# Optimization experiments

Measured on AMD Instinct MI355X. Metric: run time of the kernel, lower is better.

Reference implementation:

```python
import jax, jax.numpy as jnp
import numpy as np

E = 1024   # d_model
H = 16     # nhead
F = 4096   # dim_feedforward
EPS = 1e-5


def _ln(x, g, b):
    mu = jnp.mean(x, axis=-1, keepdims=True)
    var = jnp.mean(jnp.square(x - mu), axis=-1, keepdims=True)
    return (x - mu) * jax.lax.rsqrt(var + EPS) * g + b


def setup_inputs() -> dict:
    key = jax.random.key(0)
    ks = jax.random.split(key, 12)
    s = 0.02
    return {
        "query": jax.random.normal(ks[0], (4, 512, E), jnp.float32),
        "key_value": jax.random.normal(ks[1], (4, 2048, E), jnp.float32),
        "wq": jax.random.normal(ks[2], (E, E), jnp.float32) * s,
        "wk": jax.random.normal(ks[3], (E, E), jnp.float32) * s,
        "wv": jax.random.normal(ks[4], (E, E), jnp.float32) * s,
        "bq": jnp.zeros((E,), jnp.float32),
        "bk": jnp.zeros((E,), jnp.float32),
        "bv": jnp.zeros((E,), jnp.float32),
        "wo": jax.random.normal(ks[5], (E, E), jnp.float32) * s,
        "bo": jnp.zeros((E,), jnp.float32),
        "g1": jnp.ones((E,), jnp.float32),
        "be1": jnp.zeros((E,), jnp.float32),
        "w1": jax.random.normal(ks[6], (F, E), jnp.float32) * s,
        "b1": jnp.zeros((F,), jnp.float32),
        "w2": jax.random.normal(ks[7], (E, F), jnp.float32) * s,
        "b2": jnp.zeros((E,), jnp.float32),
        "g2": jnp.ones((E,), jnp.float32),
        "be2": jnp.zeros((E,), jnp.float32),
    }


def reference(query, key_value, wq, wk, wv, bq, bk, bv, wo, bo,
              g1, be1, w1, b1, w2, b2, g2, be2):
    B, Lq, _ = query.shape
    Lk = key_value.shape[1]
    Dh = E // H
    # projections (torch Linear: x @ W.T + b)
    q = (query @ wq.T + bq).reshape(B, Lq, H, Dh).transpose(0, 2, 1, 3)   # bhqd
    k = (key_value @ wk.T + bk).reshape(B, Lk, H, Dh).transpose(0, 2, 1, 3)
    v = (key_value @ wv.T + bv).reshape(B, Lk, H, Dh).transpose(0, 2, 1, 3)
    scores = jnp.einsum('bhqd,bhkd->bhqk', q, k) / jnp.sqrt(jnp.float32(Dh))
    attn = jax.nn.softmax(scores, axis=-1)                                # [B,H,Lq,Lk]
    ctx = jnp.einsum('bhqk,bhkd->bhqd', attn, v)
    ctx = ctx.transpose(0, 2, 1, 3).reshape(B, Lq, E)
    attn_out = ctx @ wo.T + bo
    # residual + LN1 (dropout = 0)
    q2 = _ln(query + attn_out, g1, be1)
    # FFN (ReLU activation per default)
    ffn = jax.nn.relu(q2 @ w1.T + b1) @ w2.T + b2
    q3 = _ln(q2 + ffn, g2, be2)
    return q3, attn
```

## Files before the change

kernel.cpp:

```cpp
#include <hip/hip_runtime.h>
#include <hip/hip_bf16.h>

#define E_DIM 1024
#define NHEAD 16
#define DHEAD 64
#define FDIM 4096
#define LQ 512
#define LKV 2048
#define NB 4

typedef __bf16 bfx8 __attribute__((ext_vector_type(8)));
typedef float f32x4 __attribute__((ext_vector_type(4)));
typedef unsigned short us8 __attribute__((ext_vector_type(8)));
typedef unsigned short us4 __attribute__((ext_vector_type(4)));

__device__ __forceinline__ unsigned short f2bf(float f){
  union { float f; unsigned int u; } v; v.f = f;
  unsigned int u = v.u;
  u += 0x7FFFu + ((u >> 16) & 1u);
  return (unsigned short)(u >> 16);
}

__device__ __forceinline__ float fexp2(float x){
#if __has_builtin(__builtin_amdgcn_exp2f)
  return __builtin_amdgcn_exp2f(x);
#else
  return exp2f(x);
#endif
}

__global__ __launch_bounds__(256) void cvt_kernel(const float* __restrict__ src,
                                                  unsigned short* __restrict__ dst){
  size_t i = ((size_t)blockIdx.x * 256 + threadIdx.x) * 8;
  float4 a = *reinterpret_cast<const float4*>(src + i);
  float4 b = *reinterpret_cast<const float4*>(src + i + 4);
  us8 o;
  o[0]=f2bf(a.x); o[1]=f2bf(a.y); o[2]=f2bf(a.z); o[3]=f2bf(a.w);
  o[4]=f2bf(b.x); o[5]=f2bf(b.y); o[6]=f2bf(b.z); o[7]=f2bf(b.w);
  *reinterpret_cast<us8*>(dst + i) = o;
}

template<int BN, bool HASBIAS, bool RELU, bool OUTF, bool OUTB>
__global__ __launch_bounds__(256) void gemm128(
    const unsigned short* __restrict__ A, const unsigned short* __restrict__ W,
    const float* __restrict__ bias, float* __restrict__ Cf, unsigned short* __restrict__ Cb,
    int M, int N, int K, int lda, int ldw, int ldc)
{
  constexpr int BM  = 128;
  constexpr int NFB = BN / 32;
  __shared__ unsigned short As[BM * 64];
  __shared__ unsigned short Bs[BN * 64];

  const int tid = threadIdx.x, lane = tid & 63, w = tid >> 6;
  const int wr = w >> 1, wc = w & 1;
  const int m0 = blockIdx.y * BM, n0 = blockIdx.x * BN;
  const int l15 = lane & 15, l4 = lane >> 4;

  f32x4 acc[4][NFB] = {};

  for (int k0 = 0; k0 < K; k0 += 64){
    __syncthreads();
    #pragma unroll
    for (int c = 0; c < BM/32; c++){
      const int o = (c*256 + tid) * 16;
      const int row = o >> 7, colb = o & 127;
      __builtin_amdgcn_global_load_lds(
        (const __attribute__((address_space(1))) void*)
            ((const char*)A + ((long)(m0+row)*lda + k0)*2 + colb),
        (__attribute__((address_space(3))) unsigned int*)((char*)As + o), 16, 0, 0);
    }
    #pragma unroll
    for (int c = 0; c < BN/32; c++){
      const int o = (c*256 + tid) * 16;
      const int row = o >> 7, colb = o & 127;
      __builtin_amdgcn_global_load_lds(
        (const __attribute__((address_space(1))) void*)
            ((const char*)W + ((long)(n0+row)*ldw + k0)*2 + colb),
        (__attribute__((address_space(3))) unsigned int*)((char*)Bs + o), 16, 0, 0);
    }
    __syncthreads();
    #pragma unroll
    for (int kk = 0; kk < 2; kk++){
      const int kb = kk*32 + l4*8;
      bfx8 af[4], bf[NFB];
      #pragma unroll
      for (int mi = 0; mi < 4; mi++)
        af[mi] = *reinterpret_cast<const bfx8*>(&As[(wr*64 + mi*16 + l15)*64 + kb]);
      #pragma unroll
      for (int ni = 0; ni < NFB; ni++)
        bf[ni] = *reinterpret_cast<const bfx8*>(&Bs[(wc*(BN/2) + ni*16 + l15)*64 + kb]);
      #pragma unroll
      for (int mi = 0; mi < 4; mi++)
        #pragma unroll
        for (int ni = 0; ni < NFB; ni++)
          acc[mi][ni] = __builtin_amdgcn_mfma_f32_16x16x32_bf16(af[mi], bf[ni], acc[mi][ni], 0,0,0);
    }
  }

  const int rbase = m0 + wr*64 + l4*4;
  const int cbase = n0 + wc*(BN/2) + l15;
  #pragma unroll
  for (int mi = 0; mi < 4; mi++)
  #pragma unroll
  for (int ni = 0; ni < NFB; ni++){
    const int nn = cbase + ni*16;
    float bv = 0.f;
    if constexpr (HASBIAS) bv = bias[nn];
    #pragma unroll
    for (int r = 0; r < 4; r++){
      const int mm = rbase + mi*16 + r;
      float v = acc[mi][ni][r];
      if constexpr (HASBIAS) v += bv;
      if constexpr (RELU) v = fmaxf(v, 0.f);
      const long idx = (long)mm*ldc + nn;
      if constexpr (OUTF) Cf[idx] = v;
      if constexpr (OUTB) Cb[idx] = f2bf(v);
    }
  }
}

__global__ __launch_bounds__(256) void transpose_v_kernel(const unsigned short* __restrict__ vp,
                                                          unsigned short* __restrict__ vt){
  __shared__ unsigned short T[128][66];
  const int z = blockIdx.x; const int b = z >> 4, h = z & 15;
  const int lk0 = blockIdx.y * 128;
  const int tid = threadIdx.x;
  #pragma unroll
  for (int c = 0; c < 4; c++){
    int ch = tid + c*256;
    int row = ch >> 3, col = (ch & 7) << 3;
    us8 v = *reinterpret_cast<const us8*>(vp + (long)b*LKV*E_DIM + (long)(lk0+row)*E_DIM + h*DHEAD + col);
    #pragma unroll
    for (int j = 0; j < 8; j++) T[row][col+j] = v[j];
  }
  __syncthreads();
  #pragma unroll
  for (int c = 0; c < 4; c++){
    int ch = tid + c*256;
    int d = ch >> 4, lkc = (ch & 15) << 3;
    us8 o;
    #pragma unroll
    for (int j = 0; j < 8; j++) o[j] = T[lkc+j][d];
    *reinterpret_cast<us8*>(vt + (long)z*DHEAD*LKV + (long)d*LKV + lk0 + lkc) = o;
  }
}

__global__ __launch_bounds__(256) void attn_fused(
    const unsigned short* __restrict__ qp, const unsigned short* __restrict__ kp,
    const unsigned short* __restrict__ vt, float* __restrict__ probs,
    unsigned short* __restrict__ ctx)
{
  __shared__ unsigned short Pl[4][2][16][72];

  const int hw = blockIdx.x;
  const int logical = (hw & 7)*64 + (hw >> 3);
  const int head = logical >> 3, qt = logical & 7;
  const int b = head >> 4, h = head & 15;

  const int tid = threadIdx.x, lane = tid & 63, w = tid >> 6;
  const int l15 = lane & 15, l4 = lane >> 4;
  const float SC = 0.18033688011112042f;

  const unsigned short* qb = qp + ((long)(b*LQ + qt*64 + w*16 + l15))*E_DIM + h*DHEAD + l4*8;
  bfx8 qf[2];
  qf[0] = *reinterpret_cast<const bfx8*>(qb);
  qf[1] = *reinterpret_cast<const bfx8*>(qb + 32);

  const unsigned short* kb = kp + ((long)(b*LKV) + l15)*E_DIM + h*DHEAD + l4*8;
  const unsigned short* vb = vt + ((long)head)*DHEAD*LKV + (long)l15*LKV + l4*8;

  float mloc[4] = {-1e30f,-1e30f,-1e30f,-1e30f};
  float psum[4] = {0.f,0.f,0.f,0.f};

  for (int kt = 0; kt < LKV/64; kt++){
    f32x4 s[4] = {};
    #pragma unroll
    for (int kk = 0; kk < 2; kk++)
      #pragma unroll
      for (int nf = 0; nf < 4; nf++){
        bfx8 kf = *reinterpret_cast<const bfx8*>(kb + ((long)(kt*64 + nf*16))*E_DIM + kk*32);
        s[nf] = __builtin_amdgcn_mfma_f32_16x16x32_bf16(qf[kk], kf, s[nf], 0,0,0);
      }
    #pragma unroll
    for (int r = 0; r < 4; r++){
      float nm = mloc[r];
      float e0 = s[0][r]*SC, e1 = s[1][r]*SC, e2 = s[2][r]*SC, e3 = s[3][r]*SC;
      nm = fmaxf(nm, fmaxf(fmaxf(e0,e1), fmaxf(e2,e3)));
      float add = fexp2(e0-nm) + fexp2(e1-nm) + fexp2(e2-nm) + fexp2(e3-nm);
      psum[r] = psum[r]*fexp2(mloc[r]-nm) + add;
      mloc[r] = nm;
    }
  }
  float m2[4], linv[4];
  #pragma unroll
  for (int r = 0; r < 4; r++){
    float m = mloc[r];
    m = fmaxf(m, __shfl_xor(m, 1)); m = fmaxf(m, __shfl_xor(m, 2));
    m = fmaxf(m, __shfl_xor(m, 4)); m = fmaxf(m, __shfl_xor(m, 8));
    float p = psum[r] * fexp2(mloc[r] - m);
    p += __shfl_xor(p, 1); p += __shfl_xor(p, 2);
    p += __shfl_xor(p, 4); p += __shfl_xor(p, 8);
    m2[r] = m; linv[r] = 1.f / p;
  }

  f32x4 pv[4] = {};
  float* prow = probs + ((long)head*LQ + qt*64 + w*16 + l4*4)*LKV + l15;
  for (int kt = 0; kt < LKV/64; kt++){
    f32x4 s[4] = {};
    #pragma unroll
    for (int kk = 0; kk < 2; kk++)
      #pragma unroll
      for (int nf = 0; nf < 4; nf++){
        bfx8 kf = *reinterpret_cast<const bfx8*>(kb + ((long)(kt*64 + nf*16))*E_DIM + kk*32);
        s[nf] = __builtin_amdgcn_mfma_f32_16x16x32_bf16(qf[kk], kf, s[nf], 0,0,0);
      }
    const int par = kt & 1;
    #pragma unroll
    for (int nf = 0; nf < 4; nf++)
      #pragma unroll
      for (int r = 0; r < 4; r++){
        float pr = fexp2(s[nf][r]*SC - m2[r]) * linv[r];
        prow[(long)r*LKV + kt*64 + nf*16] = pr;
        Pl[w][par][l4*4+r][nf*16+l15] = f2bf(pr);
      }
    #pragma unroll
    for (int kk = 0; kk < 2; kk++){
      bfx8 pa = *reinterpret_cast<const bfx8*>(&Pl[w][par][l15][kk*32 + l4*8]);
      #pragma unroll
      for (int nf = 0; nf < 4; nf++){
        bfx8 vf = *reinterpret_cast<const bfx8*>(vb + (long)(nf*16)*LKV + kt*64 + kk*32);
        pv[nf] = __builtin_amdgcn_mfma_f32_16x16x32_bf16(pa, vf, pv[nf], 0,0,0);
      }
    }
  }
  unsigned short* crow = ctx + ((long)(b*LQ + qt*64 + w*16 + l4*4))*E_DIM + h*DHEAD + l15;
  #pragma unroll
  for (int nf = 0; nf < 4; nf++)
    #pragma unroll
    for (int r = 0; r < 4; r++)
      crow[(long)r*E_DIM + nf*16] = f2bf(pv[nf][r]);
}

template<bool OUTB>
__global__ __launch_bounds__(256) void ln_kernel(
    const float* __restrict__ X, const float* __restrict__ Y,
    const float* __restrict__ g, const float* __restrict__ be,
    float* __restrict__ outF, unsigned short* __restrict__ outBp)
{
  __shared__ float redA[4], redB[4];
  const long base = (long)blockIdx.x * E_DIM;
  const int tid = threadIdx.x;
  float4 x = *reinterpret_cast<const float4*>(X + base + tid*4);
  float4 y = *reinterpret_cast<const float4*>(Y + base + tid*4);
  x.x += y.x; x.y += y.y; x.z += y.z; x.w += y.w;
  float s1 = x.x + x.y + x.z + x.w;
  float s2 = x.x*x.x + x.y*x.y + x.z*x.z + x.w*x.w;
  #pragma unroll
  for (int off = 32; off; off >>= 1){ s1 += __shfl_xor(s1, off); s2 += __shfl_xor(s2, off); }
  if ((tid & 63) == 0){ redA[tid>>6] = s1; redB[tid>>6] = s2; }
  __syncthreads();
  s1 = redA[0]+redA[1]+redA[2]+redA[3];
  s2 = redB[0]+redB[1]+redB[2]+redB[3];
  const float mean = s1 * (1.0f/E_DIM);
  const float var  = s2 * (1.0f/E_DIM) - mean*mean;
  const float inv  = rsqrtf(var + 1e-5f);
  float4 gv = *reinterpret_cast<const float4*>(g  + tid*4);
  float4 bv = *reinterpret_cast<const float4*>(be + tid*4);
  float4 o;
  o.x = (x.x - mean)*inv*gv.x + bv.x;
  o.y = (x.y - mean)*inv*gv.y + bv.y;
  o.z = (x.z - mean)*inv*gv.z + bv.z;
  o.w = (x.w - mean)*inv*gv.w + bv.w;
  *reinterpret_cast<float4*>(outF + base + tid*4) = o;
  if constexpr (OUTB){
    us4 ob; ob[0]=f2bf(o.x); ob[1]=f2bf(o.y); ob[2]=f2bf(o.z); ob[3]=f2bf(o.w);
    *reinterpret_cast<us4*>(outBp + base + tid*4) = ob;
  }
}

extern "C" void kernel_launch(void* const* d_in, const int* in_sizes, int n_in,
                              void* d_out, int out_size, void* d_ws, size_t ws_size,
                              hipStream_t stream)
{
  const float* query     = (const float*)d_in[0];
  const float* key_value = (const float*)d_in[1];
  const float* wq = (const float*)d_in[2];
  const float* wk = (const float*)d_in[3];
  const float* wv = (const float*)d_in[4];
  const float* bq = (const float*)d_in[5];
  const float* bk = (const float*)d_in[6];
  const float* bv = (const float*)d_in[7];
  const float* wo = (const float*)d_in[8];
  const float* bo = (const float*)d_in[9];
  const float* g1 = (const float*)d_in[10];
  const float* be1= (const float*)d_in[11];
  const float* w1 = (const float*)d_in[12];
  const float* b1 = (const float*)d_in[13];
  const float* w2 = (const float*)d_in[14];
  const float* b2 = (const float*)d_in[15];
  const float* g2 = (const float*)d_in[16];
  const float* be2= (const float*)d_in[17];

  float* q3   = (float*)d_out;
  float* attn = q3 + (size_t)NB*LQ*E_DIM;

  unsigned short* u = (unsigned short*)d_ws;
  unsigned short* xq_b  = u; u += 2097152;
  unsigned short* xkv_b = u; u += 8388608;
  unsigned short* wq_b  = u; u += 1048576;
  unsigned short* wk_b  = u; u += 1048576;
  unsigned short* wv_b  = u; u += 1048576;
  unsigned short* wo_b  = u; u += 1048576;
  unsigned short* w1_b  = u; u += 4194304;
  unsigned short* w2_b  = u; u += 4194304;
  unsigned short* qp_b  = u; u += 2097152;
  unsigned short* kp_b  = u; u += 8388608;
  unsigned short* vp_b  = u; u += 8388608;
  unsigned short* vt_b  = u; u += 8388608;
  unsigned short* ctx_b = u; u += 2097152;
  unsigned short* q2_b  = u; u += 2097152;
  float* attn_out_f = (float*)xkv_b;
  float* q2_f       = (float*)kp_b;
  float* ffn_f      = (float*)vp_b;
  unsigned short* h1_b = vt_b;

  const dim3 blk(256);

  cvt_kernel<<<dim3(1024), blk, 0, stream>>>(query, xq_b);
  cvt_kernel<<<dim3(4096), blk, 0, stream>>>(key_value, xkv_b);
  cvt_kernel<<<dim3(512),  blk, 0, stream>>>(wq, wq_b);
  cvt_kernel<<<dim3(512),  blk, 0, stream>>>(wk, wk_b);
  cvt_kernel<<<dim3(512),  blk, 0, stream>>>(wv, wv_b);
  cvt_kernel<<<dim3(512),  blk, 0, stream>>>(wo, wo_b);
  cvt_kernel<<<dim3(2048), blk, 0, stream>>>(w1, w1_b);
  cvt_kernel<<<dim3(2048), blk, 0, stream>>>(w2, w2_b);

  gemm128<64 ,true,false,false,true><<<dim3(16,16), blk, 0, stream>>>(
      xq_b, wq_b, bq, nullptr, qp_b, NB*LQ, E_DIM, E_DIM, E_DIM, E_DIM, E_DIM);
  gemm128<128,true,false,false,true><<<dim3(8,64), blk, 0, stream>>>(
      xkv_b, wk_b, bk, nullptr, kp_b, NB*LKV, E_DIM, E_DIM, E_DIM, E_DIM, E_DIM);
  gemm128<128,true,false,false,true><<<dim3(8,64), blk, 0, stream>>>(
      xkv_b, wv_b, bv, nullptr, vp_b, NB*LKV, E_DIM, E_DIM, E_DIM, E_DIM, E_DIM);

  transpose_v_kernel<<<dim3(NB*NHEAD, LKV/128), blk, 0, stream>>>(vp_b, vt_b);

  attn_fused<<<dim3(512), blk, 0, stream>>>(qp_b, kp_b, vt_b, attn, ctx_b);

  gemm128<64,true,false,true,false><<<dim3(16,16), blk, 0, stream>>>(
      ctx_b, wo_b, bo, attn_out_f, nullptr, NB*LQ, E_DIM, E_DIM, E_DIM, E_DIM, E_DIM);

  ln_kernel<true><<<dim3(NB*LQ), blk, 0, stream>>>(query, attn_out_f, g1, be1, q2_f, q2_b);

  gemm128<128,true,true,false,true><<<dim3(32,16), blk, 0, stream>>>(
      q2_b, w1_b, b1, nullptr, h1_b, NB*LQ, FDIM, E_DIM, E_DIM, E_DIM, FDIM);

  gemm128<64,true,false,true,false><<<dim3(16,16), blk, 0, stream>>>(
      h1_b, w2_b, b2, ffn_f, nullptr, NB*LQ, E_DIM, FDIM, FDIM, FDIM, E_DIM);

  ln_kernel<false><<<dim3(NB*LQ), blk, 0, stream>>>(q2_f, ffn_f, g2, be2, q3, nullptr);
}
```

Before: 770.2 us.

## Split attention key range across four wave groups with split-K softmax merge

The attention kernel now runs 1024 threads per block: 16 waves, where four groups each handle a quarter of the key/value sequence for the same 64 query rows. Per-group running max and sum are exchanged through shared memory to build the global softmax statistics, and the partial PV accumulators are reduced through shared memory, aliased onto the P buffer, before writing ctx. This is meant to raise parallelism and latency hiding in a kernel that had only 512 blocks of 4 waves. In exchange it adds barriers and shared-memory reductions, and the larger block may limit registers per thread.

New measurement: 765.8 us. About the same (-0.6%).

```diff
diff --git a/kernel.cpp b/kernel.cpp
--- a/kernel.cpp
+++ b/kernel.cpp
@@ -145,12 +145,15 @@
   }
 }
 
-__global__ __launch_bounds__(256) void attn_fused(
+__global__ __launch_bounds__(1024) void attn_fused(
     const unsigned short* __restrict__ qp, const unsigned short* __restrict__ kp,
     const unsigned short* __restrict__ vt, float* __restrict__ probs,
     unsigned short* __restrict__ ctx)
 {
-  __shared__ unsigned short Pl[4][2][16][72];
+  __shared__ unsigned short Pl[16][2][16][72];
+  __shared__ float MLm[16][16];
+  __shared__ float MLl[16][16];
+  float (*PVm)[16][64] = (float (*)[16][64])(void*)Pl;
 
   const int hw = blockIdx.x;
   const int logical = (hw & 7)*64 + (hw >> 3);
@@ -158,10 +161,12 @@
   const int b = head >> 4, h = head & 15;
 
   const int tid = threadIdx.x, lane = tid & 63, w = tid >> 6;
+  const int wq = w & 3, ws = w >> 2;
   const int l15 = lane & 15, l4 = lane >> 4;
+  const int kt0 = ws*8, kt1 = kt0 + 8;
   const float SC = 0.18033688011112042f;
 
-  const unsigned short* qb = qp + ((long)(b*LQ + qt*64 + w*16 + l15))*E_DIM + h*DHEAD + l4*8;
+  const unsigned short* qb = qp + ((long)(b*LQ + qt*64 + wq*16 + l15))*E_DIM + h*DHEAD + l4*8;
   bfx8 qf[2];
   qf[0] = *reinterpret_cast<const bfx8*>(qb);
   qf[1] = *reinterpret_cast<const bfx8*>(qb + 32);
@@ -172,7 +177,7 @@
   float mloc[4] = {-1e30f,-1e30f,-1e30f,-1e30f};
   float psum[4] = {0.f,0.f,0.f,0.f};
 
-  for (int kt = 0; kt < LKV/64; kt++){
+  for (int kt = kt0; kt < kt1; kt++){
     f32x4 s[4] = {};
     #pragma unroll
     for (int kk = 0; kk < 2; kk++)
@@ -191,7 +196,6 @@
       mloc[r] = nm;
     }
   }
-  float m2[4], linv[4];
   #pragma unroll
   for (int r = 0; r < 4; r++){
     float m = mloc[r];
@@ -200,12 +204,24 @@
     float p = psum[r] * fexp2(mloc[r] - m);
     p += __shfl_xor(p, 1); p += __shfl_xor(p, 2);
     p += __shfl_xor(p, 4); p += __shfl_xor(p, 8);
-    m2[r] = m; linv[r] = 1.f / p;
+    if (l15 == 0){ MLm[w][l4*4+r] = m; MLl[w][l4*4+r] = p; }
+  }
+  __syncthreads();
+  float m2[4], linv[4];
+  #pragma unroll
+  for (int r = 0; r < 4; r++){
+    const int row = l4*4 + r;
+    float ma = MLm[wq   ][row], mb2 = MLm[wq+ 4][row];
+    float mc = MLm[wq+ 8][row], md  = MLm[wq+12][row];
+    float mg = fmaxf(fmaxf(ma,mb2), fmaxf(mc,md));
+    float lg = MLl[wq   ][row]*fexp2(ma -mg) + MLl[wq+ 4][row]*fexp2(mb2-mg)
+             + MLl[wq+ 8][row]*fexp2(mc -mg) + MLl[wq+12][row]*fexp2(md -mg);
+    m2[r] = mg; linv[r] = 1.f / lg;
   }
 
   f32x4 pv[4] = {};
-  float* prow = probs + ((long)head*LQ + qt*64 + w*16 + l4*4)*LKV + l15;
-  for (int kt = 0; kt < LKV/64; kt++){
+  float* prow = probs + ((long)head*LQ + qt*64 + wq*16 + l4*4)*LKV + l15;
+  for (int kt = kt0; kt < kt1; kt++){
     f32x4 s[4] = {};
     #pragma unroll
     for (int kk = 0; kk < 2; kk++)
@@ -233,12 +249,35 @@
       }
     }
   }
-  unsigned short* crow = ctx + ((long)(b*LQ + qt*64 + w*16 + l4*4))*E_DIM + h*DHEAD + l15;
-  #pragma unroll
-  for (int nf = 0; nf < 4; nf++)
-    #pragma unroll
-    for (int r = 0; r < 4; r++)
-      crow[(long)r*E_DIM + nf*16] = f2bf(pv[nf][r]);
+
+  __syncthreads();
+  if (ws != 0){
+    const int i = (ws-1)*4 + wq;
+    #pragma unroll
+    for (int nf = 0; nf < 4; nf++)
+      #pragma unroll
+      for (int r = 0; r < 4; r++)
+        PVm[i][l4*4+r][nf*16+l15] = pv[nf][r];
+  }
+  __syncthreads();
+  if (ws == 0){
+    #pragma unroll
+    for (int nf = 0; nf < 4; nf++)
+      #pragma unroll
+      for (int r = 0; r < 4; r++){
+        float v = pv[nf][r];
+        v += PVm[wq  ][l4*4+r][nf*16+l15];
+        v += PVm[wq+4][l4*4+r][nf*16+l15];
+        v += PVm[wq+8][l4*4+r][nf*16+l15];
+        pv[nf][r] = v;
+      }
+    unsigned short* crow = ctx + ((long)(b*LQ + qt*64 + wq*16 + l4*4))*E_DIM + h*DHEAD + l15;
+    #pragma unroll
+    for (int nf = 0; nf < 4; nf++)
+      #pragma unroll
+      for (int r = 0; r < 4; r++)
+        crow[(long)r*E_DIM + nf*16] = f2bf(pv[nf][r]);
+  }
 }
 
 template<bool OUTB>
@@ -344,7 +383,7 @@
 
   transpose_v_kernel<<<dim3(NB*NHEAD, LKV/128), blk, 0, stream>>>(vp_b, vt_b);
 
-  attn_fused<<<dim3(512), blk, 0, stream>>>(qp_b, kp_b, vt_b, attn, ctx_b);
+  attn_fused<<<dim3(512), dim3(1024), 0, stream>>>(qp_b, kp_b, vt_b, attn, ctx_b);
 
   gemm128<64,true,false,true,false><<<dim3(16,16), blk, 0, stream>>>(
       ctx_b, wo_b, bo, attn_out_f, nullptr, NB*LQ, E_DIM, E_DIM, E_DIM, E_DIM, E_DIM);
```

## Stage K and V tiles into swizzled LDS with double-buffered async loads

Applied to the files above, without the earlier changes.

The attention kernel now loads each 64x64 K tile (and V tile in the second pass) into LDS once per block with global_load_lds, double-buffered so the next tile is prefetched during compute. The four waves share these tiles instead of each wave reading K/V fragments straight from global memory, and an XOR swizzle is meant to avoid LDS bank conflicts. This adds a block-wide barrier per tile and 32KB of LDS, which may reduce occupancy. There is no explicit wait for the async LDS loads (vmcnt) before they are consumed, so correctness depends on __syncthreads ordering those loads.

Measured after the change: 679.0 us. -11.8%, faster.

```diff
diff --git a/kernel.cpp b/kernel.cpp
--- a/kernel.cpp
+++ b/kernel.cpp
@@ -150,6 +150,8 @@
     const unsigned short* __restrict__ vt, float* __restrict__ probs,
     unsigned short* __restrict__ ctx)
 {
+  __shared__ unsigned short Ks[2][64*64];
+  __shared__ unsigned short Vs[2][64*64];
   __shared__ unsigned short Pl[4][2][16][72];
 
   const int hw = blockIdx.x;
@@ -166,21 +168,52 @@
   qf[0] = *reinterpret_cast<const bfx8*>(qb);
   qf[1] = *reinterpret_cast<const bfx8*>(qb + 32);
 
-  const unsigned short* kb = kp + ((long)(b*LKV) + l15)*E_DIM + h*DHEAD + l4*8;
-  const unsigned short* vb = vt + ((long)head)*DHEAD*LKV + (long)l15*LKV + l4*8;
+  const unsigned short* kbase = kp + (long)(b*LKV)*E_DIM + h*DHEAD;
+  const unsigned short* vbase = vt + (long)head*DHEAD*LKV;
+
+  auto stageK = [&](int kt, int buf){
+    #pragma unroll
+    for (int c = 0; c < 2; c++){
+      const int s = c*256 + tid;
+      const int row = s >> 3;
+      const int colb = ((s & 7) << 4) ^ ((row & 7) << 4);
+      __builtin_amdgcn_global_load_lds(
+        (const __attribute__((address_space(1))) void*)
+            ((const char*)(kbase + (long)(kt*64 + row)*E_DIM) + colb),
+        (__attribute__((address_space(3))) unsigned int*)((char*)&Ks[buf][0] + s*16), 16, 0, 0);
+    }
+  };
+  auto stageV = [&](int kt, int buf){
+    #pragma unroll
+    for (int c = 0; c < 2; c++){
+      const int s = c*256 + tid;
+      const int row = s >> 3;
+      const int colb = ((s & 7) << 4) ^ ((row & 7) << 4);
+      __builtin_amdgcn_global_load_lds(
+        (const __attribute__((address_space(1))) void*)
+            ((const char*)(vbase + (long)row*LKV + kt*64) + colb),
+        (__attribute__((address_space(3))) unsigned int*)((char*)&Vs[buf][0] + s*16), 16, 0, 0);
+    }
+  };
+  auto fragLds = [&](const unsigned short* base, int nf, int kk) -> bfx8 {
+    const int row = nf*16 + l15;
+    const int colb = (kk*64 + l4*16) ^ ((row & 7) << 4);
+    return *reinterpret_cast<const bfx8*>((const char*)base + row*128 + colb);
+  };
 
   float mloc[4] = {-1e30f,-1e30f,-1e30f,-1e30f};
   float psum[4] = {0.f,0.f,0.f,0.f};
 
+  stageK(0, 0);
   for (int kt = 0; kt < LKV/64; kt++){
+    __syncthreads();
+    if (kt < LKV/64 - 1) stageK(kt+1, (kt+1)&1);
     f32x4 s[4] = {};
     #pragma unroll
     for (int kk = 0; kk < 2; kk++)
       #pragma unroll
-      for (int nf = 0; nf < 4; nf++){
-        bfx8 kf = *reinterpret_cast<const bfx8*>(kb + ((long)(kt*64 + nf*16))*E_DIM + kk*32);
-        s[nf] = __builtin_amdgcn_mfma_f32_16x16x32_bf16(qf[kk], kf, s[nf], 0,0,0);
-      }
+      for (int nf = 0; nf < 4; nf++)
+        s[nf] = __builtin_amdgcn_mfma_f32_16x16x32_bf16(qf[kk], fragLds(&Ks[kt&1][0], nf, kk), s[nf], 0,0,0);
     #pragma unroll
     for (int r = 0; r < 4; r++){
       float nm = mloc[r];
@@ -205,15 +238,16 @@
 
   f32x4 pv[4] = {};
   float* prow = probs + ((long)head*LQ + qt*64 + w*16 + l4*4)*LKV + l15;
+  stageK(0, 0); stageV(0, 0);
   for (int kt = 0; kt < LKV/64; kt++){
+    __syncthreads();
+    if (kt < LKV/64 - 1){ stageK(kt+1, (kt+1)&1); stageV(kt+1, (kt+1)&1); }
     f32x4 s[4] = {};
     #pragma unroll
     for (int kk = 0; kk < 2; kk++)
       #pragma unroll
-      for (int nf = 0; nf < 4; nf++){
-        bfx8 kf = *reinterpret_cast<const bfx8*>(kb + ((long)(kt*64 + nf*16))*E_DIM + kk*32);
-        s[nf] = __builtin_amdgcn_mfma_f32_16x16x32_bf16(qf[kk], kf, s[nf], 0,0,0);
-      }
+      for (int nf = 0; nf < 4; nf++)
+        s[nf] = __builtin_amdgcn_mfma_f32_16x16x32_bf16(qf[kk], fragLds(&Ks[kt&1][0], nf, kk), s[nf], 0,0,0);
     const int par = kt & 1;
     #pragma unroll
     for (int nf = 0; nf < 4; nf++)
@@ -227,10 +261,8 @@
     for (int kk = 0; kk < 2; kk++){
       bfx8 pa = *reinterpret_cast<const bfx8*>(&Pl[w][par][l15][kk*32 + l4*8]);
       #pragma unroll
-      for (int nf = 0; nf < 4; nf++){
-        bfx8 vf = *reinterpret_cast<const bfx8*>(vb + (long)(nf*16)*LKV + kt*64 + kk*32);
-        pv[nf] = __builtin_amdgcn_mfma_f32_16x16x32_bf16(pa, vf, pv[nf], 0,0,0);
-      }
+      for (int nf = 0; nf < 4; nf++)
+        pv[nf] = __builtin_amdgcn_mfma_f32_16x16x32_bf16(pa, fragLds(&Vs[par][0], nf, kk), pv[nf], 0,0,0);
     }
   }
   unsigned short* crow = ctx + ((long)(b*LQ + qt*64 + w*16 + l4*4))*E_DIM + h*DHEAD + l15;
```
